# Kernel optimization log

Measured on AMD Instinct MI355X. Metric: run time of the kernel, lower is better.

Reference implementation:

```python
import jax, jax.numpy as jnp
import numpy as np

B, D_IN, EMB = 8192, 4000, 96
H0, H1 = 2048, 1024
NB, NC, OPT = 8, 8, 32
NE = NB * NC  # 64 experts (total contests)


def setup_inputs() -> dict:
    key = jax.random.key(0)
    ks = jax.random.split(key, 10)
    scale = lambda fan_in: jnp.sqrt(2.0 / fan_in)  # kaiming_normal-ish
    return {
        "inputs": jax.random.normal(ks[0], (B, D_IN), dtype=jnp.float32),
        "emb_table": jax.random.normal(ks[1], (NE, EMB), dtype=jnp.float32) * scale(EMB),
        "W0": jax.random.normal(ks[2], (D_IN + EMB, H0), dtype=jnp.float32) * scale(D_IN + EMB),
        "b0": jnp.zeros((H0,), dtype=jnp.float32),
        "W1": jax.random.normal(ks[3], (H0, H1), dtype=jnp.float32) * scale(H0),
        "b1": jnp.zeros((H1,), dtype=jnp.float32),
        "We": jax.random.normal(ks[4], (NE, H1, OPT), dtype=jnp.float32) * scale(H1),
        "be": jnp.zeros((NE, OPT), dtype=jnp.float32),
        "ballot_number": jax.random.randint(ks[5], (B,), 0, NB, dtype=jnp.int32),
        "contest_number": jax.random.randint(ks[6], (B,), 0, NC, dtype=jnp.int32),
        "batches": B,
    }


def reference(inputs, emb_table, W0, b0, W1, b1, We, be,
              ballot_number, contest_number, batches):
    # flat expert index per sample: index_of[ballot][contest] with equal-size ballots
    expert = ballot_number * NC + contest_number                  # [B]
    x = inputs.reshape(batches, -1)                               # [B, D_IN]
    emb = emb_table[expert]                                       # [B, EMB] (gather)
    h = jnp.concatenate([emb, x], axis=1)                         # [B, D_IN+EMB]
    h = jax.nn.relu(h @ W0 + b0)                                  # fc0 (dropout = id at eval)
    h = jax.nn.relu(h @ W1 + b1)                                  # fc1
    # per-sample routed linear: gather expert weights, batched matvec
    out = jnp.einsum("bd,bdo->bo", h, We[expert]) + be[expert]    # [B, OPT]
    return jax.nn.sigmoid(out)
```

## Files before the change

### kernel.cpp

```cpp
#include <hip/hip_runtime.h>
#include <math.h>

typedef __attribute__((ext_vector_type(8))) short short8;
typedef __attribute__((ext_vector_type(4))) float f32x4;

#define B_SZ 8192
#define D_INN 4000
#define EMBD 96
#define H0D 2048
#define H1D 1024
#define KDIM 4096

#define MFMA_BF16 __builtin_amdgcn_mfma_f32_16x16x32_bf16

__device__ __forceinline__ unsigned short f2bf(float f) {
  union { float f; unsigned u; } v; v.f = f;
  unsigned r = v.u + 0x7FFFu + ((v.u >> 16) & 1u);
  return (unsigned short)(r >> 16);
}
__device__ __forceinline__ float bf2f(unsigned short h) {
  union { unsigned u; float f; } v; v.u = ((unsigned)h) << 16;
  return v.f;
}
__device__ __forceinline__ void gld_lds16(const void* g, void* l) {
  __builtin_amdgcn_global_load_lds(
      (const __attribute__((address_space(1))) unsigned int*)g,
      (__attribute__((address_space(3))) unsigned int*)l, 16, 0, 0);
}

__global__ __launch_bounds__(256) void transpose_cvt(
    const float* __restrict__ in, unsigned short* __restrict__ out, int R, int C) {
  __shared__ float tile[32][33];
  int c0 = blockIdx.x * 32, r0 = blockIdx.y * 32;
  int tc = threadIdx.x & 31, tr = threadIdx.x >> 5;
#pragma unroll
  for (int i = 0; i < 4; ++i) {
    int r = tr + i * 8;
    tile[r][tc] = in[(size_t)(r0 + r) * C + (c0 + tc)];
  }
  __syncthreads();
#pragma unroll
  for (int i = 0; i < 4; ++i) {
    int rr = tr + i * 8;
    out[(size_t)(c0 + rr) * R + (r0 + tc)] = f2bf(tile[tc][rr]);
  }
}

__global__ __launch_bounds__(256) void transpose_cvt_we(
    const float* __restrict__ in, unsigned short* __restrict__ out) {
  __shared__ float tile[32][33];
  const int e = blockIdx.y, r0 = blockIdx.x * 32;
  const float* src = in + (size_t)e * 32768;
  unsigned short* dst = out + (size_t)e * 32768;
  int tc = threadIdx.x & 31, tr = threadIdx.x >> 5;
#pragma unroll
  for (int i = 0; i < 4; ++i) {
    int r = tr + i * 8;
    tile[r][tc] = src[(size_t)(r0 + r) * 32 + tc];
  }
  __syncthreads();
#pragma unroll
  for (int i = 0; i < 4; ++i) {
    int rr = tr + i * 8;
    dst[(size_t)rr * H1D + r0 + tc] = f2bf(tile[tc][rr]);
  }
}

__global__ __launch_bounds__(256) void build_A(
    const float* __restrict__ inputs, const float* __restrict__ emb,
    const int* __restrict__ ballot, const int* __restrict__ contest,
    unsigned short* __restrict__ A) {
  int gid = blockIdx.x * 256 + threadIdx.x;
  int b = gid >> 9, c = gid & 511;
  const float* src;
  if (c < EMBD / 8) {
    int e = ballot[b] * 8 + contest[b];
    src = emb + (size_t)e * EMBD + c * 8;
  } else {
    src = inputs + (size_t)b * D_INN + (c - EMBD / 8) * 8;
  }
  float4 v0 = *(const float4*)src;
  float4 v1 = *(const float4*)(src + 4);
  unsigned short r[8];
  r[0] = f2bf(v0.x); r[1] = f2bf(v0.y); r[2] = f2bf(v0.z); r[3] = f2bf(v0.w);
  r[4] = f2bf(v1.x); r[5] = f2bf(v1.y); r[6] = f2bf(v1.z); r[7] = f2bf(v1.w);
  *reinterpret_cast<short8*>(A + (size_t)b * KDIM + c * 8) =
      *reinterpret_cast<const short8*>(r);
}

template <int K>
__global__ __launch_bounds__(1024) void gemm_nt_16w(
    const unsigned short* __restrict__ A, const unsigned short* __restrict__ Bt,
    const float* __restrict__ bias, unsigned short* __restrict__ C,
    int N, int NBN) {
  constexpr int SLOT = 16384;
  __shared__ char lds[6 * SLOT];

  const int tid = threadIdx.x;
  const int w = tid >> 6, l = tid & 63;
  const int lr = l & 15, kg = l >> 4;
  const int wm = w >> 2, wn = w & 3;

  int swz = (blockIdx.x & 7) * ((int)gridDim.x >> 3) + ((int)blockIdx.x >> 3);
  const int bm = swz / NBN, bn = swz - bm * NBN;
  const int NT = K >> 5;

  const int srow = tid >> 2;
  const int swzsl = (tid & 3) ^ ((srow >> 1) & 3);
  const unsigned short* gaB = A + (size_t)(bm * 256 + srow) * K + swzsl * 8;
  const unsigned short* gbB = Bt + (size_t)(bn * 256 + srow) * K + swzsl * 8;

  const int xo = (kg ^ ((lr >> 1) & 3)) << 4;
  const int aoff = (wm * 64 + lr) * 64 + xo;
  const int boff = (wn * 64 + lr) * 64 + xo;

  f32x4 acc[4][4] = {};

  auto stageA = [&](int t, int rbuf) {
    gld_lds16(gaB + t * 32, lds + rbuf * SLOT + tid * 16);
  };
  auto stageB = [&](int t, int rbuf) {
    gld_lds16(gbB + t * 32, lds + 3 * SLOT + rbuf * SLOT + tid * 16);
  };

  stageA(0, 0); stageB(0, 0);
  stageA(1, 1); stageB(1, 1);
  asm volatile("s_waitcnt vmcnt(2)" ::: "memory");
  __builtin_amdgcn_s_barrier();

  int rb = 0;
  for (int t = 0; t < NT; ++t) {
    int rb2 = rb + 2; if (rb2 >= 3) rb2 -= 3;
    const char* pa = lds + rb * SLOT + aoff;
    const char* pb = lds + 3 * SLOT + rb * SLOT + boff;

    short8 a0[2], bfr[4];
#pragma unroll
    for (int mi = 0; mi < 2; ++mi) a0[mi] = *(const short8*)(pa + mi * 1024);
#pragma unroll
    for (int ni = 0; ni < 4; ++ni) bfr[ni] = *(const short8*)(pb + ni * 1024);
    if (t + 2 < NT) stageA(t + 2, rb2);
    asm volatile("s_waitcnt lgkmcnt(0)" ::: "memory");
    __builtin_amdgcn_s_barrier();
    __builtin_amdgcn_s_setprio(1);
#pragma unroll
    for (int mi = 0; mi < 2; ++mi)
#pragma unroll
      for (int ni = 0; ni < 4; ++ni)
        acc[mi][ni] = MFMA_BF16(a0[mi], bfr[ni], acc[mi][ni], 0, 0, 0);
    __builtin_amdgcn_s_setprio(0);

    short8 a1[2];
#pragma unroll
    for (int mi = 0; mi < 2; ++mi) a1[mi] = *(const short8*)(pa + (2 + mi) * 1024);
    if (t + 2 < NT) {
      stageB(t + 2, rb2);
      asm volatile("s_waitcnt lgkmcnt(0)" ::: "memory");
      asm volatile("s_waitcnt vmcnt(2)" ::: "memory");
      __builtin_amdgcn_s_barrier();
    } else if (t + 1 < NT) {
      asm volatile("s_waitcnt lgkmcnt(0)" ::: "memory");
      asm volatile("s_waitcnt vmcnt(0)" ::: "memory");
      __builtin_amdgcn_s_barrier();
    } else {
      asm volatile("s_waitcnt lgkmcnt(0)" ::: "memory");
    }
    __builtin_amdgcn_s_setprio(1);
#pragma unroll
    for (int mi = 0; mi < 2; ++mi)
#pragma unroll
      for (int ni = 0; ni < 4; ++ni)
        acc[2 + mi][ni] = MFMA_BF16(a1[mi], bfr[ni], acc[2 + mi][ni], 0, 0, 0);
    __builtin_amdgcn_s_setprio(0);

    rb = rb + 1; if (rb >= 3) rb = 0;
  }

#pragma unroll
  for (int mi = 0; mi < 4; ++mi) {
    const int row0 = bm * 256 + wm * 64 + mi * 16 + kg * 4;
#pragma unroll
    for (int ni = 0; ni < 4; ++ni) {
      const int col = bn * 256 + wn * 64 + ni * 16 + lr;
      const float bv = bias[col];
#pragma unroll
      for (int j = 0; j < 4; ++j) {
        float v = acc[mi][ni][j] + bv;
        v = v > 0.f ? v : 0.f;
        C[(size_t)(row0 + j) * N + col] = f2bf(v);
      }
    }
  }
}

template <int MREP>
__global__ __launch_bounds__(512, 2) void gemm_nt_pipe(
    const unsigned short* __restrict__ A, const unsigned short* __restrict__ Bt,
    const float* __restrict__ bias, unsigned short* __restrict__ C,
    int K, int N, int NBN) {
  constexpr int BM  = MREP * 32;
  constexpr int AI  = MREP / 4;
  constexpr int ASH = BM * 32;
  constexpr int MH  = MREP / 2;
  __shared__ unsigned short lds[3 * ASH + 3 * 8192];

  const int tid = threadIdx.x;
  const int w = tid >> 6, l = tid & 63;
  const int lr = l & 15, kg = l >> 4;
  const int wm = w >> 2, wn = w & 3;

  int swz = (blockIdx.x & 7) * ((int)gridDim.x >> 3) + ((int)blockIdx.x >> 3);
  const int bm = swz / NBN, bn = swz - bm * NBN;
  const int NT = K >> 5;

  const int rg = l >> 2;
  const int sl = ((l & 3) ^ ((l >> 3) & 3)) * 8;
  const unsigned short* ga[AI];
#pragma unroll
  for (int i = 0; i < AI; ++i)
    ga[i] = A + (size_t)(bm * BM + (i * 8 + w) * 16 + rg) * K + sl;
  const unsigned short* gb0 = Bt + (size_t)(bn * 256 + w * 16 + rg) * K + sl;
  const unsigned short* gb1 = gb0 + (size_t)128 * K;

  const int xo = (kg ^ ((lr >> 1) & 3)) << 4;
  const int aoff = (wm * (MREP * 16) + lr) * 64 + xo;
  const int boff = (wn * 64 + lr) * 64 + xo;

  f32x4 acc[MREP][4] = {};

  auto stageA = [&](int t, int rbuf) {
    unsigned short* la = lds + rbuf * ASH + w * 512;
    const int ko = t * 32;
#pragma unroll
    for (int i = 0; i < AI; ++i) gld_lds16(ga[i] + ko, la + i * 4096);
  };
  auto stageB = [&](int t, int rbuf) {
    unsigned short* lb = lds + 3 * ASH + rbuf * 8192 + w * 512;
    const int ko = t * 32;
    gld_lds16(gb0 + ko, lb);
    gld_lds16(gb1 + ko, lb + 4096);
  };

#define WAIT_VM_STEADY() do { \
    if constexpr (AI == 2) asm volatile("s_waitcnt vmcnt(4)" ::: "memory"); \
    else                   asm volatile("s_waitcnt vmcnt(3)" ::: "memory"); \
  } while (0)

  stageA(0, 0); stageB(0, 0);
  stageA(1, 1); stageB(1, 1);
  WAIT_VM_STEADY();
  __builtin_amdgcn_s_barrier();

  int rb = 0;
  for (int t = 0; t < NT; ++t) {
    int rb2 = rb + 2; if (rb2 >= 3) rb2 -= 3;
    const char* pa = (const char*)lds + rb * (ASH * 2) + aoff;
    const char* pb = (const char*)lds + 3 * (ASH * 2) + rb * 16384 + boff;

    short8 a0[MH], bfr[4];
#pragma unroll
    for (int mi = 0; mi < MH; ++mi) a0[mi] = *(const short8*)(pa + mi * 1024);
#pragma unroll
    for (int ni = 0; ni < 4; ++ni)  bfr[ni] = *(const short8*)(pb + ni * 1024);
    if (t + 2 < NT) stageA(t + 2, rb2);
    asm volatile("s_waitcnt lgkmcnt(0)" ::: "memory");
    __builtin_amdgcn_s_barrier();
    __builtin_amdgcn_s_setprio(1);
#pragma unroll
    for (int mi = 0; mi < MH; ++mi)
#pragma unroll
      for (int ni = 0; ni < 4; ++ni)
        acc[mi][ni] = MFMA_BF16(a0[mi], bfr[ni], acc[mi][ni], 0, 0, 0);
    __builtin_amdgcn_s_setprio(0);

    short8 a1[MH];
#pragma unroll
    for (int mi = 0; mi < MH; ++mi) a1[mi] = *(const short8*)(pa + (MH + mi) * 1024);
    if (t + 2 < NT) {
      stageB(t + 2, rb2);
      asm volatile("s_waitcnt lgkmcnt(0)" ::: "memory");
      WAIT_VM_STEADY();
      __builtin_amdgcn_s_barrier();
    } else if (t + 1 < NT) {
      asm volatile("s_waitcnt lgkmcnt(0)" ::: "memory");
      asm volatile("s_waitcnt vmcnt(0)" ::: "memory");
      __builtin_amdgcn_s_barrier();
    } else {
      asm volatile("s_waitcnt lgkmcnt(0)" ::: "memory");
    }
    __builtin_amdgcn_s_setprio(1);
#pragma unroll
    for (int mi = 0; mi < MH; ++mi)
#pragma unroll
      for (int ni = 0; ni < 4; ++ni)
        acc[MH + mi][ni] = MFMA_BF16(a1[mi], bfr[ni], acc[MH + mi][ni], 0, 0, 0);
    __builtin_amdgcn_s_setprio(0);

    rb = rb + 1; if (rb >= 3) rb = 0;
  }

#pragma unroll
  for (int mi = 0; mi < MREP; ++mi) {
    const int row0 = bm * BM + wm * (MREP * 16) + mi * 16 + kg * 4;
#pragma unroll
    for (int ni = 0; ni < 4; ++ni) {
      const int col = bn * 256 + wn * 64 + ni * 16 + lr;
      const float bv = bias[col];
#pragma unroll
      for (int j = 0; j < 4; ++j) {
        float v = acc[mi][ni][j] + bv;
        v = v > 0.f ? v : 0.f;
        C[(size_t)(row0 + j) * N + col] = f2bf(v);
      }
    }
  }
#undef WAIT_VM_STEADY
}

__global__ __launch_bounds__(256) void expert_head_mfma(
    const unsigned short* __restrict__ h1, const unsigned short* __restrict__ Wet,
    const float* __restrict__ be, const int* __restrict__ ballot,
    const int* __restrict__ contest, float* __restrict__ out) {
  const int e = blockIdx.x;
  __shared__ unsigned short sidx[1024];
  __shared__ int scnt;
  if (threadIdx.x == 0) scnt = 0;
  __syncthreads();
  for (int i = threadIdx.x; i < B_SZ; i += 256)
    if (ballot[i] * 8 + contest[i] == e) {
      int p = atomicAdd(&scnt, 1);
      if (p < 1024) sidx[p] = (unsigned short)i;
    }
  __syncthreads();
  const int cnt = min(scnt, 1024);
  const int w = threadIdx.x >> 6, l = threadIdx.x & 63;
  const int lr = l & 15, kg = l >> 4;
  const unsigned short* wbase = Wet + (size_t)e * 32768;
  for (int c0 = w * 32; c0 < cnt; c0 += 128) {
    const int ns = min(32, cnt - c0);
    f32x4 acc[2][2] = {};
    int ridx[2];
#pragma unroll
    for (int mi = 0; mi < 2; ++mi) {
      int rr = mi * 16 + lr;
      ridx[mi] = sidx[c0 + (rr < ns ? rr : 0)];
    }
#pragma unroll 4
    for (int kk = 0; kk < 32; ++kk) {
      short8 a0 = *(const short8*)(h1 + (size_t)ridx[0] * H1D + kk * 32 + kg * 8);
      short8 a1 = *(const short8*)(h1 + (size_t)ridx[1] * H1D + kk * 32 + kg * 8);
      short8 b0 = *(const short8*)(wbase + (size_t)lr * H1D + kk * 32 + kg * 8);
      short8 b1 = *(const short8*)(wbase + (size_t)(16 + lr) * H1D + kk * 32 + kg * 8);
      acc[0][0] = MFMA_BF16(a0, b0, acc[0][0], 0, 0, 0);
      acc[0][1] = MFMA_BF16(a0, b1, acc[0][1], 0, 0, 0);
      acc[1][0] = MFMA_BF16(a1, b0, acc[1][0], 0, 0, 0);
      acc[1][1] = MFMA_BF16(a1, b1, acc[1][1], 0, 0, 0);
    }
#pragma unroll
    for (int mi = 0; mi < 2; ++mi)
#pragma unroll
      for (int ni = 0; ni < 2; ++ni)
#pragma unroll
        for (int j = 0; j < 4; ++j) {
          int row = mi * 16 + kg * 4 + j;
          int col = ni * 16 + lr;
          if (row < ns) {
            float x = acc[mi][ni][j] + be[e * 32 + col];
            out[(size_t)sidx[c0 + row] * 32 + col] = 1.f / (1.f + expf(-x));
          }
        }
  }
}

extern "C" void kernel_launch(void* const* d_in, const int* in_sizes, int n_in,
                              void* d_out, int out_size, void* d_ws, size_t ws_size,
                              hipStream_t stream) {
  const float* inputs = (const float*)d_in[0];
  const float* emb    = (const float*)d_in[1];
  const float* W0     = (const float*)d_in[2];
  const float* b0     = (const float*)d_in[3];
  const float* W1     = (const float*)d_in[4];
  const float* b1     = (const float*)d_in[5];
  const float* We     = (const float*)d_in[6];
  const float* be     = (const float*)d_in[7];
  const int* ballot   = (const int*)d_in[8];
  const int* contest  = (const int*)d_in[9];
  float* out = (float*)d_out;

  char* ws = (char*)d_ws;
  unsigned short* A   = (unsigned short*)(ws);
  unsigned short* W0t = (unsigned short*)(ws + 67108864);
  unsigned short* h0  = (unsigned short*)(ws + 83886080);
  unsigned short* W1t = (unsigned short*)(ws + 117440512);
  unsigned short* h1  = (unsigned short*)(ws + 121634816);
  unsigned short* Wet = (unsigned short*)(ws);

  dim3 blk(256);
  transpose_cvt<<<dim3(H0D / 32, KDIM / 32, 1), blk, 0, stream>>>(W0, W0t, KDIM, H0D);
  transpose_cvt<<<dim3(H1D / 32, H0D / 32, 1), blk, 0, stream>>>(W1, W1t, H0D, H1D);
  build_A<<<dim3(B_SZ * 512 / 256), blk, 0, stream>>>(inputs, emb, ballot, contest, A);
  gemm_nt_16w<KDIM><<<dim3(256), dim3(1024), 0, stream>>>(A, W0t, b0, h0, H0D, H0D / 256);
  transpose_cvt_we<<<dim3(32, 64), blk, 0, stream>>>(We, Wet);
  gemm_nt_pipe<4><<<dim3((B_SZ / 128) * (H1D / 256)), dim3(512), 0, stream>>>(
      h0, W1t, b1, h1, H0D, H1D, H1D / 256);
  expert_head_mfma<<<dim3(64), blk, 0, stream>>>(h1, Wet, be, ballot, contest, out);
}
```

Measured before the change: 242.8 us.

## Drop mid-iteration barriers in fc0 GEMM and add 16-wave fc1 GEMM

In the fc0 GEMM main loop, the LDS-wait plus barrier after issuing the A prefetch is removed. The B prefetch now overlaps the second MFMA half, leaving only one barrier per K step. The fc1 GEMM is replaced by a dedicated 1024-thread kernel with a 128x256 tile and a 64-wide K stage, using a triple-buffered XOR-swizzled LDS layout. Each thread issues a single combined A+B stage per step. The aim is fewer synchronisation stalls and more MFMA work per barrier. The cost is higher LDS use and a reliance on the remaining barrier to keep buffer reuse safe.

Measured after the change: 235.7 us. -2.9%, faster.

```diff
diff --git a/kernel.cpp b/kernel.cpp
--- a/kernel.cpp
+++ b/kernel.cpp
@@ -140,8 +140,6 @@
 #pragma unroll
     for (int ni = 0; ni < 4; ++ni) bfr[ni] = *(const short8*)(pb + ni * 1024);
     if (t + 2 < NT) stageA(t + 2, rb2);
-    asm volatile("s_waitcnt lgkmcnt(0)" ::: "memory");
-    __builtin_amdgcn_s_barrier();
     __builtin_amdgcn_s_setprio(1);
 #pragma unroll
     for (int mi = 0; mi < 2; ++mi)
@@ -153,26 +151,22 @@
     short8 a1[2];
 #pragma unroll
     for (int mi = 0; mi < 2; ++mi) a1[mi] = *(const short8*)(pa + (2 + mi) * 1024);
+    if (t + 2 < NT) stageB(t + 2, rb2);
+    __builtin_amdgcn_s_setprio(1);
+#pragma unroll
+    for (int mi = 0; mi < 2; ++mi)
+#pragma unroll
+      for (int ni = 0; ni < 4; ++ni)
+        acc[2 + mi][ni] = MFMA_BF16(a1[mi], bfr[ni], acc[2 + mi][ni], 0, 0, 0);
+    __builtin_amdgcn_s_setprio(0);
+
     if (t + 2 < NT) {
-      stageB(t + 2, rb2);
-      asm volatile("s_waitcnt lgkmcnt(0)" ::: "memory");
       asm volatile("s_waitcnt vmcnt(2)" ::: "memory");
       __builtin_amdgcn_s_barrier();
     } else if (t + 1 < NT) {
-      asm volatile("s_waitcnt lgkmcnt(0)" ::: "memory");
       asm volatile("s_waitcnt vmcnt(0)" ::: "memory");
       __builtin_amdgcn_s_barrier();
-    } else {
-      asm volatile("s_waitcnt lgkmcnt(0)" ::: "memory");
-    }
-    __builtin_amdgcn_s_setprio(1);
-#pragma unroll
-    for (int mi = 0; mi < 2; ++mi)
-#pragma unroll
-      for (int ni = 0; ni < 4; ++ni)
-        acc[2 + mi][ni] = MFMA_BF16(a1[mi], bfr[ni], acc[2 + mi][ni], 0, 0, 0);
-    __builtin_amdgcn_s_setprio(0);
-
+    }
     rb = rb + 1; if (rb >= 3) rb = 0;
   }
 
@@ -193,16 +187,13 @@
   }
 }
 
-template <int MREP>
-__global__ __launch_bounds__(512, 2) void gemm_nt_pipe(
+__global__ __launch_bounds__(1024) void gemm2_16w(
     const unsigned short* __restrict__ A, const unsigned short* __restrict__ Bt,
-    const float* __restrict__ bias, unsigned short* __restrict__ C,
-    int K, int N, int NBN) {
-  constexpr int BM  = MREP * 32;
-  constexpr int AI  = MREP / 4;
-  constexpr int ASH = BM * 32;
-  constexpr int MH  = MREP / 2;
-  __shared__ unsigned short lds[3 * ASH + 3 * 8192];
+    const float* __restrict__ bias, unsigned short* __restrict__ C) {
+  constexpr int K = H0D, N = H1D, NBN = 4;
+  constexpr int ASLOT = 16384, BSLOT = 32768;
+  constexpr int NT = K / 64;
+  __shared__ char lds[3 * ASLOT + 3 * BSLOT];
 
   const int tid = threadIdx.x;
   const int w = tid >> 6, l = tid & 63;
@@ -211,97 +202,72 @@
 
   int swz = (blockIdx.x & 7) * ((int)gridDim.x >> 3) + ((int)blockIdx.x >> 3);
   const int bm = swz / NBN, bn = swz - bm * NBN;
-  const int NT = K >> 5;
-
-  const int rg = l >> 2;
-  const int sl = ((l & 3) ^ ((l >> 3) & 3)) * 8;
-  const unsigned short* ga[AI];
-#pragma unroll
-  for (int i = 0; i < AI; ++i)
-    ga[i] = A + (size_t)(bm * BM + (i * 8 + w) * 16 + rg) * K + sl;
-  const unsigned short* gb0 = Bt + (size_t)(bn * 256 + w * 16 + rg) * K + sl;
+
+  const int srow = tid >> 3;
+  const int sslot = (tid & 7) ^ (srow & 7);
+  const unsigned short* gaB = A + (size_t)(bm * 128 + srow) * K + sslot * 8;
+  const unsigned short* gb0 = Bt + (size_t)(bn * 256 + srow) * K + sslot * 8;
   const unsigned short* gb1 = gb0 + (size_t)128 * K;
 
-  const int xo = (kg ^ ((lr >> 1) & 3)) << 4;
-  const int aoff = (wm * (MREP * 16) + lr) * 64 + xo;
-  const int boff = (wn * 64 + lr) * 64 + xo;
-
-  f32x4 acc[MREP][4] = {};
-
-  auto stageA = [&](int t, int rbuf) {
-    unsigned short* la = lds + rbuf * ASH + w * 512;
-    const int ko = t * 32;
-#pragma unroll
-    for (int i = 0; i < AI; ++i) gld_lds16(ga[i] + ko, la + i * 4096);
+  f32x4 acc[2][4] = {};
+
+  auto stage = [&](int t, int rbuf) {
+    gld_lds16(gaB + t * 64, lds + rbuf * ASLOT + tid * 16);
+    char* lb = lds + 3 * ASLOT + rbuf * BSLOT + tid * 16;
+    gld_lds16(gb0 + t * 64, lb);
+    gld_lds16(gb1 + t * 64, lb + 16384);
   };
-  auto stageB = [&](int t, int rbuf) {
-    unsigned short* lb = lds + 3 * ASH + rbuf * 8192 + w * 512;
-    const int ko = t * 32;
-    gld_lds16(gb0 + ko, lb);
-    gld_lds16(gb1 + ko, lb + 4096);
+
+  auto rdrow = [&](const char* base, int row, int ks) -> short8 {
+    return *(const short8*)(base + row * 128 + (((ks << 2) | kg) ^ (row & 7)) * 16);
   };
 
-#define WAIT_VM_STEADY() do { \
-    if constexpr (AI == 2) asm volatile("s_waitcnt vmcnt(4)" ::: "memory"); \
-    else                   asm volatile("s_waitcnt vmcnt(3)" ::: "memory"); \
-  } while (0)
-
-  stageA(0, 0); stageB(0, 0);
-  stageA(1, 1); stageB(1, 1);
-  WAIT_VM_STEADY();
+  stage(0, 0);
+  stage(1, 1);
+  asm volatile("s_waitcnt vmcnt(3)" ::: "memory");
   __builtin_amdgcn_s_barrier();
 
   int rb = 0;
   for (int t = 0; t < NT; ++t) {
     int rb2 = rb + 2; if (rb2 >= 3) rb2 -= 3;
-    const char* pa = (const char*)lds + rb * (ASH * 2) + aoff;
-    const char* pb = (const char*)lds + 3 * (ASH * 2) + rb * 16384 + boff;
-
-    short8 a0[MH], bfr[4];
-#pragma unroll
-    for (int mi = 0; mi < MH; ++mi) a0[mi] = *(const short8*)(pa + mi * 1024);
-#pragma unroll
-    for (int ni = 0; ni < 4; ++ni)  bfr[ni] = *(const short8*)(pb + ni * 1024);
-    if (t + 2 < NT) stageA(t + 2, rb2);
-    asm volatile("s_waitcnt lgkmcnt(0)" ::: "memory");
-    __builtin_amdgcn_s_barrier();
+    const char* pa = lds + rb * ASLOT;
+    const char* pb = lds + 3 * ASLOT + rb * BSLOT;
+
+    short8 a[2][2], b[4][2];
+#pragma unroll
+    for (int mi = 0; mi < 2; ++mi)
+#pragma unroll
+      for (int ks = 0; ks < 2; ++ks)
+        a[mi][ks] = rdrow(pa, wm * 32 + mi * 16 + lr, ks);
+#pragma unroll
+    for (int ni = 0; ni < 4; ++ni)
+#pragma unroll
+      for (int ks = 0; ks < 2; ++ks)
+        b[ni][ks] = rdrow(pb, wn * 64 + ni * 16 + lr, ks);
+    if (t + 2 < NT) stage(t + 2, rb2);
     __builtin_amdgcn_s_setprio(1);
 #pragma unroll
-    for (int mi = 0; mi < MH; ++mi)
+    for (int mi = 0; mi < 2; ++mi)
 #pragma unroll
       for (int ni = 0; ni < 4; ++ni)
-        acc[mi][ni] = MFMA_BF16(a0[mi], bfr[ni], acc[mi][ni], 0, 0, 0);
+#pragma unroll
+        for (int ks = 0; ks < 2; ++ks)
+          acc[mi][ni] = MFMA_BF16(a[mi][ks], b[ni][ks], acc[mi][ni], 0, 0, 0);
     __builtin_amdgcn_s_setprio(0);
 
-    short8 a1[MH];
-#pragma unroll
-    for (int mi = 0; mi < MH; ++mi) a1[mi] = *(const short8*)(pa + (MH + mi) * 1024);
     if (t + 2 < NT) {
-      stageB(t + 2, rb2);
-      asm volatile("s_waitcnt lgkmcnt(0)" ::: "memory");
-      WAIT_VM_STEADY();
+      asm volatile("s_waitcnt vmcnt(3)" ::: "memory");
       __builtin_amdgcn_s_barrier();
     } else if (t + 1 < NT) {
-      asm volatile("s_waitcnt lgkmcnt(0)" ::: "memory");
       asm volatile("s_waitcnt vmcnt(0)" ::: "memory");
       __builtin_amdgcn_s_barrier();
-    } else {
-      asm volatile("s_waitcnt lgkmcnt(0)" ::: "memory");
-    }
-    __builtin_amdgcn_s_setprio(1);
-#pragma unroll
-    for (int mi = 0; mi < MH; ++mi)
-#pragma unroll
-      for (int ni = 0; ni < 4; ++ni)
-        acc[MH + mi][ni] = MFMA_BF16(a1[mi], bfr[ni], acc[MH + mi][ni], 0, 0, 0);
-    __builtin_amdgcn_s_setprio(0);
-
+    }
     rb = rb + 1; if (rb >= 3) rb = 0;
   }
 
 #pragma unroll
-  for (int mi = 0; mi < MREP; ++mi) {
-    const int row0 = bm * BM + wm * (MREP * 16) + mi * 16 + kg * 4;
+  for (int mi = 0; mi < 2; ++mi) {
+    const int row0 = bm * 128 + wm * 32 + mi * 16 + kg * 4;
 #pragma unroll
     for (int ni = 0; ni < 4; ++ni) {
       const int col = bn * 256 + wn * 64 + ni * 16 + lr;
@@ -314,7 +280,6 @@
       }
     }
   }
-#undef WAIT_VM_STEADY
 }
 
 __global__ __launch_bounds__(256) void expert_head_mfma(
@@ -401,7 +366,6 @@
   build_A<<<dim3(B_SZ * 512 / 256), blk, 0, stream>>>(inputs, emb, ballot, contest, A);
   gemm_nt_16w<KDIM><<<dim3(256), dim3(1024), 0, stream>>>(A, W0t, b0, h0, H0D, H0D / 256);
   transpose_cvt_we<<<dim3(32, 64), blk, 0, stream>>>(We, Wet);
-  gemm_nt_pipe<4><<<dim3((B_SZ / 128) * (H1D / 256)), dim3(512), 0, stream>>>(
-      h0, W1t, b1, h1, H0D, H1D, H1D / 256);
+  gemm2_16w<<<dim3(256), dim3(1024), 0, stream>>>(h0, W1t, b1, h1);
   expert_head_mfma<<<dim3(64), blk, 0, stream>>>(h1, Wet, be, ballot, contest, out);
 }
```
